# Kernel optimization log

Measured on AMD Instinct MI355X. Metric: run time of the kernel, lower is better.

Reference implementation:

```python
import jax, jax.numpy as jnp
import numpy as np

N_NODES = 100_000
N_EDGES = 1_600_000
F_IN = 128
HID = 64
C_OUT = 16


def setup_inputs() -> dict:
    key = jax.random.key(0)
    k1, k2, k3, k4, k5 = jax.random.split(key, 5)
    x = jax.random.normal(k1, (N_NODES, F_IN), dtype=jnp.float32)
    edge_index = jax.random.randint(k2, (2, N_EDGES), 0, N_NODES, dtype=jnp.int64)
    edge_weight = jax.random.uniform(k3, (N_EDGES,), dtype=jnp.float32)
    # Glorot-ish init for the two GCNConv linear layers; PyG inits bias to zero.
    W1 = jax.random.normal(k4, (F_IN, HID), dtype=jnp.float32) * (1.0 / np.sqrt(F_IN))
    b1 = jnp.zeros((HID,), dtype=jnp.float32)
    W2 = jax.random.normal(k5, (HID, C_OUT), dtype=jnp.float32) * (1.0 / np.sqrt(HID))
    b2 = jnp.zeros((C_OUT,), dtype=jnp.float32)
    return {"x": x, "edge_index": edge_index, "edge_weight": edge_weight,
            "W1": W1, "b1": b1, "W2": W2, "b2": b2}


def gcn_layer(x, row, col, ew, W, b, n):
    """PyG GCNConv: h = D^-1/2 (A + I) D^-1/2 (x W) + b, with edge weights.
    Self loops (weight 1) are handled analytically instead of appending edges."""
    h = x @ W  # [n, out]
    deg = jax.ops.segment_sum(ew, col, num_segments=n) + 1.0  # +1 for self loop
    dinv = jax.lax.rsqrt(deg)  # deg >= 1 always
    norm = dinv[row] * ew * dinv[col]  # [E]
    agg = jax.ops.segment_sum(norm[:, None] * h[row], col, num_segments=n)
    return agg + (dinv * dinv)[:, None] * h + b


def reference(x, edge_index, edge_weight, W1, b1, W2, b2):
    row, col = edge_index[0], edge_index[1]
    h = jax.nn.relu(gcn_layer(x, row, col, edge_weight, W1, b1, N_NODES))
    # delete_min_weighted_edges(node=0): remove the min-weight edge with source 0.
    # Zeroing its weight is mathematically identical to deleting it (it then
    # contributes 0 to both the degree and the aggregation).
    masked = jnp.where(row == 0, edge_weight, jnp.inf)
    idx = jnp.argmin(masked)
    ew2 = edge_weight.at[idx].set(0.0)
    return gcn_layer(h, row, col, ew2, W2, b2, N_NODES)
```

## Files before the change

kernel.cpp:

```cpp
#include <hip/hip_runtime.h>
#include <hip/hip_bf16.h>
#include <stdint.h>

#define NN 100000
#define NE 1600000
#define FIN 128
#define HID 64
#define COUT 16

#define BUKSH 8
#define BUKN 256
#define NBUK ((NN + BUKN - 1) >> BUKSH)
#define CAP 5120
#define PART_NB 200
#define EPB (NE / PART_NB)

typedef unsigned long long u64;
typedef short bf16x8 __attribute__((ext_vector_type(8)));
typedef float f32x4 __attribute__((ext_vector_type(4)));

struct Flags { int f32; int i64; };

__device__ __forceinline__ float b2f(__hip_bfloat16 v) { return __bfloat162float(v); }

__device__ __forceinline__ float ldf(const void* p, size_t i, int f32) {
    return f32 ? ((const float*)p)[i]
               : __bfloat162float(((const __hip_bfloat16*)p)[i]);
}
__device__ __forceinline__ int lde(const void* p, size_t i, int i64) {
    return i64 ? (int)((const long long*)p)[i] : ((const int*)p)[i];
}
__device__ __forceinline__ void ld4bf(const __hip_bfloat16* p, float& x0, float& x1,
                                      float& x2, float& x3) {
    union { uint2 u; __hip_bfloat16 h[4]; } v;
    v.u = *(const uint2*)p;
    x0 = b2f(v.h[0]); x1 = b2f(v.h[1]); x2 = b2f(v.h[2]); x3 = b2f(v.h[3]);
}
__device__ __forceinline__ unsigned short f2bfu(float f) {
    union { __hip_bfloat16 b; unsigned short u; } c;
    c.b = __float2bfloat16(f);
    return c.u;
}
__device__ __forceinline__ float bfu2f(unsigned short u) {
    union { unsigned short h[2]; float f; } c;
    c.h[0] = 0; c.h[1] = u;
    return c.f;
}

__global__ __launch_bounds__(256) void k_init(const unsigned short* xs,
                                              const int* ei32, Flags* fl,
                                              int* cursorA, u64* minkey,
                                              int* delpos) {
    int t = threadIdx.x;
    if (t < 64) {
        int lane = t;
        int huge = 0;
        for (int i = lane * 2; i < 1024; i += 128) {
            int e = (xs[i] >> 7) & 0xFF;
            if (e >= 0xC0) huge = 1;
        }
        int odd_nonzero = 0;
        for (int i = 1 + lane * 2; i < 512; i += 128) {
            if (ei32[i] != 0) odd_nonzero = 1;
        }
        u64 h = __ballot(huge), o = __ballot(odd_nonzero);
        if (lane == 0) { fl->f32 = (h != 0); fl->i64 = (o == 0); }
    }
    for (int i = t; i < NBUK; i += 256) cursorA[i] = 0;
    if (t == 64) *minkey = ~0ull;
    if (t == 65) *delpos = -1;
}

__global__ void k_mink(const void* __restrict__ ei, const void* __restrict__ ew,
                       const Flags* __restrict__ fl, u64* __restrict__ minkey) {
    int e = blockIdx.x * blockDim.x + threadIdx.x;
    if (e >= NE) return;
    int r = lde(ei, e, fl->i64);
    if (r == 0) {
        float w = ldf(ew, e, fl->f32);
        u64 key = ((u64)__float_as_uint(w) << 32) | (unsigned)e;
        atomicMin(minkey, key);
    }
}

__global__ __launch_bounds__(256) void k_partA(const void* __restrict__ ei,
                                               const void* __restrict__ ew,
                                               const Flags* __restrict__ fl,
                                               const u64* __restrict__ minkey,
                                               int* __restrict__ cursorA,
                                               long long* __restrict__ tmp) {
    __shared__ int cnt[NBUK];
    __shared__ int base[NBUK];
    int b = blockIdx.x, t = threadIdx.x;
    int f32 = fl->f32, i64 = fl->i64;
    for (int i = t; i < NBUK; i += 256) cnt[i] = 0;
    __syncthreads();
    int e0 = b * EPB;
    for (int i = t; i < EPB; i += 256) {
        int c = lde(ei, (size_t)NE + e0 + i, i64);
        atomicAdd(&cnt[c >> BUKSH], 1);
    }
    __syncthreads();
    for (int i = t; i < NBUK; i += 256) {
        int n = cnt[i];
        base[i] = n ? atomicAdd(&cursorA[i], n) : 0;
    }
    __syncthreads();
    for (int i = t; i < NBUK; i += 256) cnt[i] = 0;
    __syncthreads();
    u64 k = *minkey;
    int eidx = (k == ~0ull) ? 0 : (int)(k & 0xffffffffu);
    for (int i = t; i < EPB; i += 256) {
        int e = e0 + i;
        int r = lde(ei, e, i64);
        int c = lde(ei, (size_t)NE + e, i64);
        float w = ldf(ew, e, f32);
        int buk = c >> BUKSH;
        int slot = base[buk] + atomicAdd(&cnt[buk], 1);
        if (slot < CAP) {
            unsigned lo = (unsigned)r | (((unsigned)c & 255u) << 17)
                        | ((e == eidx) ? (1u << 25) : 0u);
            tmp[(size_t)buk * CAP + slot] = ((long long)__float_as_int(w) << 32) | lo;
        }
    }
}

__global__ __launch_bounds__(512) void k_scanBk(const int* __restrict__ cursorA,
                                                int* __restrict__ bucketBase,
                                                int* __restrict__ rowptrN) {
    __shared__ int sm[512];
    int t = threadIdx.x;
    int v = 0;
    if (t < NBUK) { v = cursorA[t]; if (v > CAP) v = CAP; }
    sm[t] = v;
    for (int off = 1; off < 512; off <<= 1) {
        __syncthreads();
        int add = (t >= off) ? sm[t - off] : 0;
        __syncthreads();
        sm[t] += add;
    }
    __syncthreads();
    if (t < NBUK) bucketBase[t] = sm[t] - v;
    if (t == 511) rowptrN[NN] = sm[511];
}

__global__ __launch_bounds__(256) void k_partB(const int* __restrict__ cursorA,
                                               const int* __restrict__ bucketBase,
                                               const long long* __restrict__ tmp,
                                               int2* __restrict__ epack,
                                               int* __restrict__ rowptrN,
                                               const void* __restrict__ ei,
                                               const void* __restrict__ ew,
                                               const Flags* __restrict__ fl,
                                               const u64* __restrict__ minkey,
                                               float* __restrict__ dinv1,
                                               float* __restrict__ dinv2,
                                               int* __restrict__ delpos) {
    __shared__ int cnt[256];
    __shared__ int pfx[256];
    __shared__ u64 wsum[256];
    int b = blockIdx.x, t = threadIdx.x;
    cnt[t] = 0; wsum[t] = 0;
    __syncthreads();
    int count = cursorA[b]; if (count > CAP) count = CAP;
    const long long* ts = tmp + (size_t)b * CAP;
    for (int i = t; i < count; i += 256) {
        long long pk = ts[i];
        unsigned lo = (unsigned)pk;
        int nl = (int)((lo >> 17) & 255u);
        atomicAdd(&cnt[nl], 1);
        float w = __int_as_float((int)(pk >> 32));
        atomicAdd(&wsum[nl], (u64)((double)w * 4294967296.0));
    }
    __syncthreads();
    int v = cnt[t];
    pfx[t] = v;
    for (int off = 1; off < 256; off <<= 1) {
        __syncthreads();
        int add = (t >= off) ? pfx[t - off] : 0;
        __syncthreads();
        pfx[t] += add;
    }
    __syncthreads();
    int excl = pfx[t] - v;
    int gbase = bucketBase[b];
    int node = (b << BUKSH) + t;
    if (node < NN) {
        rowptrN[node] = gbase + excl;
        float degv = (float)((double)wsum[t] * (1.0 / 4294967296.0));
        u64 kk = *minkey;
        int eidx = (kk == ~0ull) ? 0 : (int)(kk & 0xffffffffu);
        int cmin = lde(ei, (size_t)NE + eidx, fl->i64);
        float wmin = ldf(ew, eidx, fl->f32);
        float d1 = degv + 1.0f;
        float d2 = d1 - ((node == cmin) ? wmin : 0.0f);
        dinv1[node] = rsqrtf(d1);
        dinv2[node] = rsqrtf(d2);
    }
    __syncthreads();
    cnt[t] = gbase + excl;
    __syncthreads();
    for (int i = t; i < count; i += 256) {
        long long pk = ts[i];
        unsigned lo = (unsigned)pk;
        int nl = (int)((lo >> 17) & 255u);
        int pos = atomicAdd(&cnt[nl], 1);
        long long outpk = (pk & 0xFFFFFFFF00000000LL) | (lo & 0x1FFFFu);
        *(long long*)(epack + pos) = outpk;
        if (lo & (1u << 25)) *delpos = pos;
    }
}

__global__ __launch_bounds__(256, 3) void k_gemm1_split(const float* __restrict__ x,
                                                        const float* __restrict__ W1,
                                                        const Flags* __restrict__ fl,
                                                        const float* __restrict__ dinv1,
                                                        __hip_bfloat16* __restrict__ h1) {
    if (!fl->f32) return;
    __shared__ __align__(16) unsigned short Whi[8192];
    __shared__ __align__(16) unsigned short Wlo[8192];
    int t = threadIdx.x;
    for (int i = t; i < 8192; i += 256) {
        int k = i >> 6;
        int n = i & 63;
        int kc = k >> 5, kr = k & 31;
        int q = kr >> 3, j = kr & 7;
        int n0 = n >> 4, col = n & 15;
        float w = W1[i];
        unsigned short hi = f2bfu(w);
        unsigned short lo = f2bfu(w - bfu2f(hi));
        int idx = ((n0 << 4) + (kc << 2) + q) * 128 + col * 8 + j;
        Whi[idx] = hi;
        Wlo[idx] = lo;
    }
    __syncthreads();
    int wave = t >> 6, lane = t & 63;
    int quad = lane >> 4, col = lane & 15;
    bf16x8 Bh[4][4];
#pragma unroll
    for (int n0 = 0; n0 < 4; ++n0)
#pragma unroll
        for (int kc = 0; kc < 4; ++kc)
            Bh[kc][n0] = *(const bf16x8*)&Whi[((n0 << 4) + (kc << 2) + quad) * 128 + col * 8];
    int tile0 = (blockIdx.x * 4 + wave) * 2;
#pragma unroll 1
    for (int i = 0; i < 2; ++i) {
        int node0 = (tile0 + i) * 16;
        if (node0 >= NN) return;
        const float* xp = x + (size_t)(node0 + col) * FIN + quad * 8;
        float4 xv[8];
#pragma unroll
        for (int kc = 0; kc < 4; ++kc) {
            xv[2 * kc]     = *(const float4*)(xp + kc * 32);
            xv[2 * kc + 1] = *(const float4*)(xp + kc * 32 + 4);
        }
        f32x4 a0 = {0.f, 0.f, 0.f, 0.f}, a1 = a0, a2 = a0, a3 = a0;
#pragma unroll
        for (int kc = 0; kc < 4; ++kc) {
            float fv[8];
            fv[0] = xv[2 * kc].x;     fv[1] = xv[2 * kc].y;
            fv[2] = xv[2 * kc].z;     fv[3] = xv[2 * kc].w;
            fv[4] = xv[2 * kc + 1].x; fv[5] = xv[2 * kc + 1].y;
            fv[6] = xv[2 * kc + 1].z; fv[7] = xv[2 * kc + 1].w;
            bf16x8 Ah, Al;
#pragma unroll
            for (int j = 0; j < 8; ++j) {
                unsigned short hi = f2bfu(fv[j]);
                Ah[j] = (short)hi;
                Al[j] = (short)f2bfu(fv[j] - bfu2f(hi));
            }
            int lbase = ((kc << 2) + quad) * 128 + col * 8;
            bf16x8 Bl0 = *(const bf16x8*)&Wlo[lbase];
            bf16x8 Bl1 = *(const bf16x8*)&Wlo[(1 << 4) * 128 + lbase];
            bf16x8 Bl2 = *(const bf16x8*)&Wlo[(2 << 4) * 128 + lbase];
            bf16x8 Bl3 = *(const bf16x8*)&Wlo[(3 << 4) * 128 + lbase];
            a0 = __builtin_amdgcn_mfma_f32_16x16x32_bf16(Ah, Bh[kc][0], a0, 0, 0, 0);
            a0 = __builtin_amdgcn_mfma_f32_16x16x32_bf16(Al, Bh[kc][0], a0, 0, 0, 0);
            a0 = __builtin_amdgcn_mfma_f32_16x16x32_bf16(Ah, Bl0,      a0, 0, 0, 0);
            a1 = __builtin_amdgcn_mfma_f32_16x16x32_bf16(Ah, Bh[kc][1], a1, 0, 0, 0);
            a1 = __builtin_amdgcn_mfma_f32_16x16x32_bf16(Al, Bh[kc][1], a1, 0, 0, 0);
            a1 = __builtin_amdgcn_mfma_f32_16x16x32_bf16(Ah, Bl1,      a1, 0, 0, 0);
            a2 = __builtin_amdgcn_mfma_f32_16x16x32_bf16(Ah, Bh[kc][2], a2, 0, 0, 0);
            a2 = __builtin_amdgcn_mfma_f32_16x16x32_bf16(Al, Bh[kc][2], a2, 0, 0, 0);
            a2 = __builtin_amdgcn_mfma_f32_16x16x32_bf16(Ah, Bl2,      a2, 0, 0, 0);
            a3 = __builtin_amdgcn_mfma_f32_16x16x32_bf16(Ah, Bh[kc][3], a3, 0, 0, 0);
            a3 = __builtin_amdgcn_mfma_f32_16x16x32_bf16(Al, Bh[kc][3], a3, 0, 0, 0);
            a3 = __builtin_amdgcn_mfma_f32_16x16x32_bf16(Ah, Bl3,      a3, 0, 0, 0);
        }
        __hip_bfloat16* hp = h1 + (size_t)(node0 + quad * 4) * HID + col;
#pragma unroll
        for (int r = 0; r < 4; ++r) {
            float dsc = dinv1[node0 + quad * 4 + r];
            hp[(size_t)r * HID + 0]  = __float2bfloat16(a0[r] * dsc);
            hp[(size_t)r * HID + 16] = __float2bfloat16(a1[r] * dsc);
            hp[(size_t)r * HID + 32] = __float2bfloat16(a2[r] * dsc);
            hp[(size_t)r * HID + 48] = __float2bfloat16(a3[r] * dsc);
        }
    }
}

__global__ __launch_bounds__(256) void k_gemm1_mfma(const __hip_bfloat16* __restrict__ x,
                                                    const unsigned short* __restrict__ W1,
                                                    const Flags* __restrict__ fl,
                                                    const float* __restrict__ dinv1,
                                                    __hip_bfloat16* __restrict__ h1) {
    if (fl->f32) return;
    __shared__ __align__(16) unsigned short Wf[8192];
    int t = threadIdx.x;
    for (int i = t; i < 8192; i += 256) {
        int k = i >> 6;
        int n = i & 63;
        int kc = k >> 5, kr = k & 31;
        int q = kr >> 3, j = kr & 7;
        int n0 = n >> 4, col = n & 15;
        Wf[((((n0 << 2) | kc) << 2) | q) * 128 + col * 8 + j] = W1[i];
    }
    __syncthreads();
    int wave = t >> 6, lane = t & 63;
    int quad = lane >> 4, col = lane & 15;
    bf16x8 B[4][4];
#pragma unroll
    for (int n0 = 0; n0 < 4; ++n0)
#pragma unroll
        for (int kc = 0; kc < 4; ++kc)
            B[kc][n0] = *(const bf16x8*)&Wf[((((n0 << 2) | kc) << 2) | quad) * 128 + col * 8];
    int tile0 = (blockIdx.x * 4 + wave) * 4;
#pragma unroll 1
    for (int i = 0; i < 4; ++i) {
        int node0 = (tile0 + i) * 16;
        if (node0 >= NN) return;
        const __hip_bfloat16* xp = x + (size_t)(node0 + col) * FIN + quad * 8;
        f32x4 a0 = {0.f, 0.f, 0.f, 0.f}, a1 = a0, a2 = a0, a3 = a0;
#pragma unroll
        for (int kc = 0; kc < 4; ++kc) {
            bf16x8 A = *(const bf16x8*)(xp + kc * 32);
            a0 = __builtin_amdgcn_mfma_f32_16x16x32_bf16(A, B[kc][0], a0, 0, 0, 0);
            a1 = __builtin_amdgcn_mfma_f32_16x16x32_bf16(A, B[kc][1], a1, 0, 0, 0);
            a2 = __builtin_amdgcn_mfma_f32_16x16x32_bf16(A, B[kc][2], a2, 0, 0, 0);
            a3 = __builtin_amdgcn_mfma_f32_16x16x32_bf16(A, B[kc][3], a3, 0, 0, 0);
        }
        __hip_bfloat16* hp = h1 + (size_t)(node0 + quad * 4) * HID + col;
#pragma unroll
        for (int r = 0; r < 4; ++r) {
            float dsc = dinv1[node0 + quad * 4 + r];
            hp[(size_t)r * HID + 0]  = __float2bfloat16(a0[r] * dsc);
            hp[(size_t)r * HID + 16] = __float2bfloat16(a1[r] * dsc);
            hp[(size_t)r * HID + 32] = __float2bfloat16(a2[r] * dsc);
            hp[(size_t)r * HID + 48] = __float2bfloat16(a3[r] * dsc);
        }
    }
}

__global__ __launch_bounds__(256) void k_agg1(const int* __restrict__ rowptrN,
                                              const int2* __restrict__ epack,
                                              const float* __restrict__ dinv1,
                                              const __hip_bfloat16* __restrict__ h1,
                                              const void* __restrict__ b1,
                                              const void* __restrict__ W2,
                                              const Flags* __restrict__ fl,
                                              const float* __restrict__ dinv2,
                                              float* __restrict__ h2) {
    __shared__ float Ws[HID * COUT];
    __shared__ float obuf[16][68];
    int t = threadIdx.x;
    int f32 = fl->f32;
    for (int i = t; i < HID * COUT; i += 256) Ws[i] = ldf(W2, i, f32);
    int nn = t >> 4;
    int n = blockIdx.x * 16 + nn;
    int l = t & 15;
    int f = l * 4;
    int wbase = t & 48;
    float dn = dinv1[n];
    int p0 = rowptrN[n], p1 = rowptrN[n + 1];
    float a0 = 0.f, a1 = 0.f, a2 = 0.f, a3 = 0.f;
    for (int p = p0; p < p1; p += 16) {
        int idx = p + l;
        int2 ev = make_int2(0, 0);
        if (idx < p1) ev = epack[idx];
        float cw = __int_as_float(ev.y);
        int rj[16];
#pragma unroll
        for (int j = 0; j < 16; ++j)
            rj[j] = __shfl(ev.x, wbase + j);
        uint2 raw[16];
#pragma unroll
        for (int j = 0; j < 16; ++j)
            raw[j] = *(const uint2*)(h1 + (size_t)rj[j] * HID + f);
#pragma unroll
        for (int j = 0; j < 16; ++j) {
            float c = __shfl(cw, wbase + j);
            union { uint2 u; __hip_bfloat16 h[4]; } v; v.u = raw[j];
            a0 += c * b2f(v.h[0]);
            a1 += c * b2f(v.h[1]);
            a2 += c * b2f(v.h[2]);
            a3 += c * b2f(v.h[3]);
        }
    }
    float x0, x1, x2, x3;
    ld4bf(h1 + (size_t)n * HID + f, x0, x1, x2, x3);
    float4 o;
    o.x = fmaxf(dn * (a0 + x0) + ldf(b1, f + 0, f32), 0.f);
    o.y = fmaxf(dn * (a1 + x1) + ldf(b1, f + 1, f32), 0.f);
    o.z = fmaxf(dn * (a2 + x2) + ldf(b1, f + 2, f32), 0.f);
    o.w = fmaxf(dn * (a3 + x3) + ldf(b1, f + 3, f32), 0.f);
    obuf[nn][f + 0] = o.x; obuf[nn][f + 1] = o.y;
    obuf[nn][f + 2] = o.z; obuf[nn][f + 3] = o.w;
    __syncthreads();
    int c = t & 15;
    const float* orow = obuf[nn];
    float acc = 0.f;
#pragma unroll 8
    for (int k = 0; k < HID; ++k)
        acc += orow[k] * Ws[k * COUT + c];
    h2[(size_t)n * COUT + c] = acc * dinv2[n];
}

__global__ __launch_bounds__(256) void k_agg2(const int* __restrict__ rowptrN,
                                              const int2* __restrict__ epack,
                                              const float* __restrict__ dinv2,
                                              const float* __restrict__ h2,
                                              const void* __restrict__ bias2,
                                              const Flags* __restrict__ fl,
                                              const int* __restrict__ delpos,
                                              void* __restrict__ out) {
    int t = threadIdx.x;
    int n = blockIdx.x * 64 + (t >> 2);
    if (n >= NN) return;
    int l = t & 3;
    int f = l * 4;
    int wbase = t & 60;
    int f32 = fl->f32;
    int dp = *delpos;
    float dn = dinv2[n];
    int p0 = rowptrN[n], p1 = rowptrN[n + 1];
    float a0 = 0.f, a1 = 0.f, a2 = 0.f, a3 = 0.f;
    for (int p = p0; p < p1; p += 8) {
        int iA = p + l, iB = p + 4 + l;
        int2 evA = make_int2(0, 0), evB = make_int2(0, 0);
        if (iA < p1) evA = epack[iA];
        if (iB < p1) evB = epack[iB];
        float cwA = (iA == dp) ? 0.f : __int_as_float(evA.y);
        float cwB = (iB == dp) ? 0.f : __int_as_float(evB.y);
        int rj[8];
#pragma unroll
        for (int j = 0; j < 4; ++j) {
            rj[j]     = __shfl(evA.x, wbase + j);
            rj[4 + j] = __shfl(evB.x, wbase + j);
        }
        float4 hv[8];
#pragma unroll
        for (int j = 0; j < 8; ++j)
            hv[j] = *(const float4*)(h2 + (size_t)rj[j] * COUT + f);
#pragma unroll
        for (int j = 0; j < 4; ++j) {
            float cA = __shfl(cwA, wbase + j);
            float cB = __shfl(cwB, wbase + j);
            a0 += cA * hv[j].x + cB * hv[4 + j].x;
            a1 += cA * hv[j].y + cB * hv[4 + j].y;
            a2 += cA * hv[j].z + cB * hv[4 + j].z;
            a3 += cA * hv[j].w + cB * hv[4 + j].w;
        }
    }
    const float4 hn = *(const float4*)(h2 + (size_t)n * COUT + f);
    float o0 = dn * (a0 + hn.x) + ldf(bias2, f + 0, f32);
    float o1 = dn * (a1 + hn.y) + ldf(bias2, f + 1, f32);
    float o2 = dn * (a2 + hn.z) + ldf(bias2, f + 2, f32);
    float o3 = dn * (a3 + hn.w) + ldf(bias2, f + 3, f32);
    size_t idx = (size_t)n * COUT + f;
    if (f32) {
        float* op = (float*)out + idx;
        op[0] = o0; op[1] = o1; op[2] = o2; op[3] = o3;
    } else {
        union { uint2 u; __hip_bfloat16 h[4]; } pk;
        pk.h[0] = __float2bfloat16(o0); pk.h[1] = __float2bfloat16(o1);
        pk.h[2] = __float2bfloat16(o2); pk.h[3] = __float2bfloat16(o3);
        *(uint2*)((__hip_bfloat16*)out + idx) = pk.u;
    }
}

extern "C" void kernel_launch(void* const* d_in, const int* in_sizes, int n_in,
                              void* d_out, int out_size, void* d_ws, size_t ws_size,
                              hipStream_t stream) {
    const void* x  = d_in[0];
    const void* ei = d_in[1];
    const void* ew = d_in[2];
    const void* W1 = d_in[3];
    const void* b1 = d_in[4];
    const void* W2 = d_in[5];
    const void* b2 = d_in[6];

    char* wsb = (char*)d_ws;
    float* dinv1    = (float*)wsb;                     wsb += (size_t)NN * 4;
    float* dinv2    = (float*)wsb;                     wsb += (size_t)NN * 4;
    int*   rowptrN  = (int*)wsb;                       wsb += (size_t)(NN + 1) * 4;
    int*   cursorA  = (int*)wsb;                       wsb += (size_t)NBUK * 4;
    int*   bucketBase = (int*)wsb;                     wsb += (size_t)NBUK * 4;
    wsb = (char*)(((uintptr_t)wsb + 15) & ~(uintptr_t)15);
    int2*  epack    = (int2*)wsb;                      wsb += (size_t)NE * 8;
    __hip_bfloat16* h1 = (__hip_bfloat16*)wsb;         wsb += (size_t)NN * HID * 2;
    float* h2       = (float*)wsb;                     wsb += (size_t)NN * COUT * 4;
    long long* tmp  = (long long*)wsb;                 wsb += (size_t)NBUK * CAP * 8;
    u64*   minkey   = (u64*)wsb;                       wsb += 8;
    Flags* fl       = (Flags*)wsb;                     wsb += 8;
    int*   delpos   = (int*)wsb;                       wsb += 8;

    k_init<<<1, 256, 0, stream>>>((const unsigned short*)x, (const int*)ei, fl,
                                  cursorA, minkey, delpos);
    k_mink<<<(NE + 255) / 256, 256, 0, stream>>>(ei, ew, fl, minkey);
    k_partA<<<PART_NB, 256, 0, stream>>>(ei, ew, fl, minkey, cursorA, tmp);
    k_scanBk<<<1, 512, 0, stream>>>(cursorA, bucketBase, rowptrN);
    k_partB<<<NBUK, 256, 0, stream>>>(cursorA, bucketBase, tmp, epack, rowptrN,
                                      ei, ew, fl, minkey, dinv1, dinv2, delpos);
    k_gemm1_split<<<(NN / 16 + 7) / 8, 256, 0, stream>>>((const float*)x,
                                                         (const float*)W1, fl,
                                                         dinv1, h1);
    k_gemm1_mfma<<<(NN / 16 + 15) / 16, 256, 0, stream>>>((const __hip_bfloat16*)x,
                                                          (const unsigned short*)W1, fl,
                                                          dinv1, h1);
    k_agg1<<<NN / 16, 256, 0, stream>>>(rowptrN, epack, dinv1, h1, b1, W2, fl,
                                        dinv2, h2);
    k_agg2<<<(NN + 63) / 64, 256, 0, stream>>>(rowptrN, epack, dinv2, h2, b2, fl,
                                               delpos, d_out);
}
```

Baseline: 255.2 us.

## Fold bucket scan into partB, merge gemm kernels, widen agg1 loads

```diff
diff --git a/kernel.cpp b/kernel.cpp
--- a/kernel.cpp
+++ b/kernel.cpp
@@ -29,12 +29,6 @@
 }
 __device__ __forceinline__ int lde(const void* p, size_t i, int i64) {
     return i64 ? (int)((const long long*)p)[i] : ((const int*)p)[i];
-}
-__device__ __forceinline__ void ld4bf(const __hip_bfloat16* p, float& x0, float& x1,
-                                      float& x2, float& x3) {
-    union { uint2 u; __hip_bfloat16 h[4]; } v;
-    v.u = *(const uint2*)p;
-    x0 = b2f(v.h[0]); x1 = b2f(v.h[1]); x2 = b2f(v.h[2]); x3 = b2f(v.h[3]);
 }
 __device__ __forceinline__ unsigned short f2bfu(float f) {
     union { __hip_bfloat16 b; unsigned short u; } c;
@@ -68,7 +62,7 @@
     }
     for (int i = t; i < NBUK; i += 256) cursorA[i] = 0;
     if (t == 64) *minkey = ~0ull;
-    if (t == 65) *delpos = -1;
+    if (t == 65) *delpos = 0x7fffffff;
 }
 
 __global__ void k_mink(const void* __restrict__ ei, const void* __restrict__ ew,
@@ -86,7 +80,6 @@
 __global__ __launch_bounds__(256) void k_partA(const void* __restrict__ ei,
                                                const void* __restrict__ ew,
                                                const Flags* __restrict__ fl,
-                                               const u64* __restrict__ minkey,
                                                int* __restrict__ cursorA,
                                                long long* __restrict__ tmp) {
     __shared__ int cnt[NBUK];
@@ -108,8 +101,6 @@
     __syncthreads();
     for (int i = t; i < NBUK; i += 256) cnt[i] = 0;
     __syncthreads();
-    u64 k = *minkey;
-    int eidx = (k == ~0ull) ? 0 : (int)(k & 0xffffffffu);
     for (int i = t; i < EPB; i += 256) {
         int e = e0 + i;
         int r = lde(ei, e, i64);
@@ -118,34 +109,14 @@
         int buk = c >> BUKSH;
         int slot = base[buk] + atomicAdd(&cnt[buk], 1);
         if (slot < CAP) {
-            unsigned lo = (unsigned)r | (((unsigned)c & 255u) << 17)
-                        | ((e == eidx) ? (1u << 25) : 0u);
-            tmp[(size_t)buk * CAP + slot] = ((long long)__float_as_int(w) << 32) | lo;
-        }
-    }
-}
-
-__global__ __launch_bounds__(512) void k_scanBk(const int* __restrict__ cursorA,
-                                                int* __restrict__ bucketBase,
-                                                int* __restrict__ rowptrN) {
-    __shared__ int sm[512];
-    int t = threadIdx.x;
-    int v = 0;
-    if (t < NBUK) { v = cursorA[t]; if (v > CAP) v = CAP; }
-    sm[t] = v;
-    for (int off = 1; off < 512; off <<= 1) {
-        __syncthreads();
-        int add = (t >= off) ? sm[t - off] : 0;
-        __syncthreads();
-        sm[t] += add;
-    }
-    __syncthreads();
-    if (t < NBUK) bucketBase[t] = sm[t] - v;
-    if (t == 511) rowptrN[NN] = sm[511];
+            unsigned lo = (unsigned)r | (((unsigned)c & 255u) << 17);
+            long long rec = ((long long)__float_as_int(w) << 32) | lo;
+            __builtin_nontemporal_store(rec, &tmp[(size_t)buk * CAP + slot]);
+        }
+    }
 }
 
 __global__ __launch_bounds__(256) void k_partB(const int* __restrict__ cursorA,
-                                               const int* __restrict__ bucketBase,
                                                const long long* __restrict__ tmp,
                                                int2* __restrict__ epack,
                                                int* __restrict__ rowptrN,
@@ -160,12 +131,33 @@
     __shared__ int pfx[256];
     __shared__ u64 wsum[256];
     int b = blockIdx.x, t = threadIdx.x;
+    int partial = 0;
+    for (int i = t; i < NBUK; i += 256) {
+        int cc = cursorA[i]; if (cc > CAP) cc = CAP;
+        if (i < b) partial += cc;
+    }
+    pfx[t] = partial;
+    __syncthreads();
+    for (int off = 128; off > 0; off >>= 1) {
+        if (t < off) pfx[t] += pfx[t + off];
+        __syncthreads();
+    }
+    int gbase = pfx[0];
+    __syncthreads();
     cnt[t] = 0; wsum[t] = 0;
     __syncthreads();
     int count = cursorA[b]; if (count > CAP) count = CAP;
+    if (b == NBUK - 1 && t == 0) rowptrN[NN] = gbase + count;
+    u64 kk = *minkey;
+    int eidx = (kk == ~0ull) ? 0 : (int)(kk & 0xffffffffu);
+    int smin  = lde(ei, (size_t)eidx, fl->i64);
+    int cmin  = lde(ei, (size_t)NE + eidx, fl->i64);
+    int wminb = __float_as_int(ldf(ew, eidx, fl->f32));
+    bool myb = (b == (cmin >> BUKSH));
+    int clow = cmin & 255;
     const long long* ts = tmp + (size_t)b * CAP;
     for (int i = t; i < count; i += 256) {
-        long long pk = ts[i];
+        long long pk = __builtin_nontemporal_load(&ts[i]);
         unsigned lo = (unsigned)pk;
         int nl = (int)((lo >> 17) & 255u);
         atomicAdd(&cnt[nl], 1);
@@ -183,17 +175,12 @@
     }
     __syncthreads();
     int excl = pfx[t] - v;
-    int gbase = bucketBase[b];
     int node = (b << BUKSH) + t;
     if (node < NN) {
         rowptrN[node] = gbase + excl;
         float degv = (float)((double)wsum[t] * (1.0 / 4294967296.0));
-        u64 kk = *minkey;
-        int eidx = (kk == ~0ull) ? 0 : (int)(kk & 0xffffffffu);
-        int cmin = lde(ei, (size_t)NE + eidx, fl->i64);
-        float wmin = ldf(ew, eidx, fl->f32);
         float d1 = degv + 1.0f;
-        float d2 = d1 - ((node == cmin) ? wmin : 0.0f);
+        float d2 = d1 - ((node == cmin) ? __int_as_float(wminb) : 0.0f);
         dinv1[node] = rsqrtf(d1);
         dinv2[node] = rsqrtf(d2);
     }
@@ -201,152 +188,150 @@
     cnt[t] = gbase + excl;
     __syncthreads();
     for (int i = t; i < count; i += 256) {
-        long long pk = ts[i];
+        long long pk = __builtin_nontemporal_load(&ts[i]);
         unsigned lo = (unsigned)pk;
         int nl = (int)((lo >> 17) & 255u);
         int pos = atomicAdd(&cnt[nl], 1);
         long long outpk = (pk & 0xFFFFFFFF00000000LL) | (lo & 0x1FFFFu);
         *(long long*)(epack + pos) = outpk;
-        if (lo & (1u << 25)) *delpos = pos;
-    }
-}
-
-__global__ __launch_bounds__(256, 3) void k_gemm1_split(const float* __restrict__ x,
-                                                        const float* __restrict__ W1,
-                                                        const Flags* __restrict__ fl,
-                                                        const float* __restrict__ dinv1,
-                                                        __hip_bfloat16* __restrict__ h1) {
-    if (!fl->f32) return;
-    __shared__ __align__(16) unsigned short Whi[8192];
-    __shared__ __align__(16) unsigned short Wlo[8192];
+        if (myb && nl == clow && (int)(lo & 0x1FFFFu) == smin
+            && (int)(pk >> 32) == wminb)
+            atomicMin(delpos, pos);
+    }
+}
+
+__global__ __launch_bounds__(256, 3) void k_gemm1(const void* __restrict__ xv_,
+                                                  const void* __restrict__ W1_,
+                                                  const Flags* __restrict__ fl,
+                                                  const float* __restrict__ dinv1,
+                                                  __hip_bfloat16* __restrict__ h1) {
+    __shared__ __align__(16) unsigned short Wbuf[16384];
     int t = threadIdx.x;
-    for (int i = t; i < 8192; i += 256) {
-        int k = i >> 6;
-        int n = i & 63;
-        int kc = k >> 5, kr = k & 31;
-        int q = kr >> 3, j = kr & 7;
-        int n0 = n >> 4, col = n & 15;
-        float w = W1[i];
-        unsigned short hi = f2bfu(w);
-        unsigned short lo = f2bfu(w - bfu2f(hi));
-        int idx = ((n0 << 4) + (kc << 2) + q) * 128 + col * 8 + j;
-        Whi[idx] = hi;
-        Wlo[idx] = lo;
-    }
-    __syncthreads();
     int wave = t >> 6, lane = t & 63;
     int quad = lane >> 4, col = lane & 15;
-    bf16x8 Bh[4][4];
-#pragma unroll
-    for (int n0 = 0; n0 < 4; ++n0)
-#pragma unroll
-        for (int kc = 0; kc < 4; ++kc)
-            Bh[kc][n0] = *(const bf16x8*)&Whi[((n0 << 4) + (kc << 2) + quad) * 128 + col * 8];
-    int tile0 = (blockIdx.x * 4 + wave) * 2;
+    if (fl->f32) {
+        const float* x  = (const float*)xv_;
+        const float* W1 = (const float*)W1_;
+        unsigned short* Whi = Wbuf;
+        unsigned short* Wlo = Wbuf + 8192;
+        for (int i = t; i < 8192; i += 256) {
+            int k = i >> 6;
+            int n = i & 63;
+            int kc = k >> 5, kr = k & 31;
+            int q = kr >> 3, j = kr & 7;
+            int n0 = n >> 4, c2 = n & 15;
+            float w = W1[i];
+            unsigned short hi = f2bfu(w);
+            unsigned short lo = f2bfu(w - bfu2f(hi));
+            int idx = ((n0 << 4) + (kc << 2) + q) * 128 + c2 * 8 + j;
+            Whi[idx] = hi;
+            Wlo[idx] = lo;
+        }
+        __syncthreads();
+        bf16x8 Bh[4][4];
+#pragma unroll
+        for (int n0 = 0; n0 < 4; ++n0)
+#pragma unroll
+            for (int kc = 0; kc < 4; ++kc)
+                Bh[kc][n0] = *(const bf16x8*)&Whi[((n0 << 4) + (kc << 2) + quad) * 128 + col * 8];
+        int tile0 = (blockIdx.x * 4 + wave) * 2;
 #pragma unroll 1
-    for (int i = 0; i < 2; ++i) {
-        int node0 = (tile0 + i) * 16;
-        if (node0 >= NN) return;
-        const float* xp = x + (size_t)(node0 + col) * FIN + quad * 8;
-        float4 xv[8];
-#pragma unroll
-        for (int kc = 0; kc < 4; ++kc) {
-            xv[2 * kc]     = *(const float4*)(xp + kc * 32);
-            xv[2 * kc + 1] = *(const float4*)(xp + kc * 32 + 4);
-        }
-        f32x4 a0 = {0.f, 0.f, 0.f, 0.f}, a1 = a0, a2 = a0, a3 = a0;
-#pragma unroll
-        for (int kc = 0; kc < 4; ++kc) {
-            float fv[8];
-            fv[0] = xv[2 * kc].x;     fv[1] = xv[2 * kc].y;
-            fv[2] = xv[2 * kc].z;     fv[3] = xv[2 * kc].w;
-            fv[4] = xv[2 * kc + 1].x; fv[5] = xv[2 * kc + 1].y;
-            fv[6] = xv[2 * kc + 1].z; fv[7] = xv[2 * kc + 1].w;
-            bf16x8 Ah, Al;
-#pragma unroll
-            for (int j = 0; j < 8; ++j) {
-                unsigned short hi = f2bfu(fv[j]);
-                Ah[j] = (short)hi;
-                Al[j] = (short)f2bfu(fv[j] - bfu2f(hi));
+        for (int i = 0; i < 2; ++i) {
+            int node0 = (tile0 + i) * 16;
+            if (node0 >= NN) return;
+            const float* xp = x + (size_t)(node0 + col) * FIN + quad * 8;
+            float4 xv[8];
+#pragma unroll
+            for (int kc = 0; kc < 4; ++kc) {
+                xv[2 * kc]     = *(const float4*)(xp + kc * 32);
+                xv[2 * kc + 1] = *(const float4*)(xp + kc * 32 + 4);
             }
-            int lbase = ((kc << 2) + quad) * 128 + col * 8;
-            bf16x8 Bl0 = *(const bf16x8*)&Wlo[lbase];
-            bf16x8 Bl1 = *(const bf16x8*)&Wlo[(1 << 4) * 128 + lbase];
-            bf16x8 Bl2 = *(const bf16x8*)&Wlo[(2 << 4) * 128 + lbase];
-            bf16x8 Bl3 = *(const bf16x8*)&Wlo[(3 << 4) * 128 + lbase];
-            a0 = __builtin_amdgcn_mfma_f32_16x16x32_bf16(Ah, Bh[kc][0], a0, 0, 0, 0);
-            a0 = __builtin_amdgcn_mfma_f32_16x16x32_bf16(Al, Bh[kc][0], a0, 0, 0, 0);
-            a0 = __builtin_amdgcn_mfma_f32_16x16x32_bf16(Ah, Bl0,      a0, 0, 0, 0);
-            a1 = __builtin_amdgcn_mfma_f32_16x16x32_bf16(Ah, Bh[kc][1], a1, 0, 0, 0);
-            a1 = __builtin_amdgcn_mfma_f32_16x16x32_bf16(Al, Bh[kc][1], a1, 0, 0, 0);
-            a1 = __builtin_amdgcn_mfma_f32_16x16x32_bf16(Ah, Bl1,      a1, 0, 0, 0);
-            a2 = __builtin_amdgcn_mfma_f32_16x16x32_bf16(Ah, Bh[kc][2], a2, 0, 0, 0);
-            a2 = __builtin_amdgcn_mfma_f32_16x16x32_bf16(Al, Bh[kc][2], a2, 0, 0, 0);
-            a2 = __builtin_amdgcn_mfma_f32_16x16x32_bf16(Ah, Bl2,      a2, 0, 0, 0);
-            a3 = __builtin_amdgcn_mfma_f32_16x16x32_bf16(Ah, Bh[kc][3], a3, 0, 0, 0);
-            a3 = __builtin_amdgcn_mfma_f32_16x16x32_bf16(Al, Bh[kc][3], a3, 0, 0, 0);
-            a3 = __builtin_amdgcn_mfma_f32_16x16x32_bf16(Ah, Bl3,      a3, 0, 0, 0);
-        }
-        __hip_bfloat16* hp = h1 + (size_t)(node0 + quad * 4) * HID + col;
-#pragma unroll
-        for (int r = 0; r < 4; ++r) {
-            float dsc = dinv1[node0 + quad * 4 + r];
-            hp[(size_t)r * HID + 0]  = __float2bfloat16(a0[r] * dsc);
-            hp[(size_t)r * HID + 16] = __float2bfloat16(a1[r] * dsc);
-            hp[(size_t)r * HID + 32] = __float2bfloat16(a2[r] * dsc);
-            hp[(size_t)r * HID + 48] = __float2bfloat16(a3[r] * dsc);
-        }
-    }
-}
-
-__global__ __launch_bounds__(256) void k_gemm1_mfma(const __hip_bfloat16* __restrict__ x,
-                                                    const unsigned short* __restrict__ W1,
-                                                    const Flags* __restrict__ fl,
-                                                    const float* __restrict__ dinv1,
-                                                    __hip_bfloat16* __restrict__ h1) {
-    if (fl->f32) return;
-    __shared__ __align__(16) unsigned short Wf[8192];
-    int t = threadIdx.x;
-    for (int i = t; i < 8192; i += 256) {
-        int k = i >> 6;
-        int n = i & 63;
-        int kc = k >> 5, kr = k & 31;
-        int q = kr >> 3, j = kr & 7;
-        int n0 = n >> 4, col = n & 15;
-        Wf[((((n0 << 2) | kc) << 2) | q) * 128 + col * 8 + j] = W1[i];
-    }
-    __syncthreads();
-    int wave = t >> 6, lane = t & 63;
-    int quad = lane >> 4, col = lane & 15;
-    bf16x8 B[4][4];
-#pragma unroll
-    for (int n0 = 0; n0 < 4; ++n0)
-#pragma unroll
-        for (int kc = 0; kc < 4; ++kc)
-            B[kc][n0] = *(const bf16x8*)&Wf[((((n0 << 2) | kc) << 2) | quad) * 128 + col * 8];
-    int tile0 = (blockIdx.x * 4 + wave) * 4;
+            f32x4 a0 = {0.f, 0.f, 0.f, 0.f}, a1 = a0, a2 = a0, a3 = a0;
+#pragma unroll
+            for (int kc = 0; kc < 4; ++kc) {
+                float fv[8];
+                fv[0] = xv[2 * kc].x;     fv[1] = xv[2 * kc].y;
+                fv[2] = xv[2 * kc].z;     fv[3] = xv[2 * kc].w;
+                fv[4] = xv[2 * kc + 1].x; fv[5] = xv[2 * kc + 1].y;
+                fv[6] = xv[2 * kc + 1].z; fv[7] = xv[2 * kc + 1].w;
+                bf16x8 Ah, Al;
+#pragma unroll
+                for (int j = 0; j < 8; ++j) {
+                    unsigned short hi = f2bfu(fv[j]);
+                    Ah[j] = (short)hi;
+                    Al[j] = (short)f2bfu(fv[j] - bfu2f(hi));
+                }
+                int lbase = ((kc << 2) + quad) * 128 + col * 8;
+                bf16x8 Bl0 = *(const bf16x8*)&Wlo[lbase];
+                bf16x8 Bl1 = *(const bf16x8*)&Wlo[(1 << 4) * 128 + lbase];
+                bf16x8 Bl2 = *(const bf16x8*)&Wlo[(2 << 4) * 128 + lbase];
+                bf16x8 Bl3 = *(const bf16x8*)&Wlo[(3 << 4) * 128 + lbase];
+                a0 = __builtin_amdgcn_mfma_f32_16x16x32_bf16(Ah, Bh[kc][0], a0, 0, 0, 0);
+                a0 = __builtin_amdgcn_mfma_f32_16x16x32_bf16(Al, Bh[kc][0], a0, 0, 0, 0);
+                a0 = __builtin_amdgcn_mfma_f32_16x16x32_bf16(Ah, Bl0,      a0, 0, 0, 0);
+                a1 = __builtin_amdgcn_mfma_f32_16x16x32_bf16(Ah, Bh[kc][1], a1, 0, 0, 0);
+                a1 = __builtin_amdgcn_mfma_f32_16x16x32_bf16(Al, Bh[kc][1], a1, 0, 0, 0);
+                a1 = __builtin_amdgcn_mfma_f32_16x16x32_bf16(Ah, Bl1,      a1, 0, 0, 0);
+                a2 = __builtin_amdgcn_mfma_f32_16x16x32_bf16(Ah, Bh[kc][2], a2, 0, 0, 0);
+                a2 = __builtin_amdgcn_mfma_f32_16x16x32_bf16(Al, Bh[kc][2], a2, 0, 0, 0);
+                a2 = __builtin_amdgcn_mfma_f32_16x16x32_bf16(Ah, Bl2,      a2, 0, 0, 0);
+                a3 = __builtin_amdgcn_mfma_f32_16x16x32_bf16(Ah, Bh[kc][3], a3, 0, 0, 0);
+                a3 = __builtin_amdgcn_mfma_f32_16x16x32_bf16(Al, Bh[kc][3], a3, 0, 0, 0);
+                a3 = __builtin_amdgcn_mfma_f32_16x16x32_bf16(Ah, Bl3,      a3, 0, 0, 0);
+            }
+            __hip_bfloat16* hp = h1 + (size_t)(node0 + quad * 4) * HID + col;
+#pragma unroll
+            for (int r = 0; r < 4; ++r) {
+                float dsc = dinv1[node0 + quad * 4 + r];
+                hp[(size_t)r * HID + 0]  = __float2bfloat16(a0[r] * dsc);
+                hp[(size_t)r * HID + 16] = __float2bfloat16(a1[r] * dsc);
+                hp[(size_t)r * HID + 32] = __float2bfloat16(a2[r] * dsc);
+                hp[(size_t)r * HID + 48] = __float2bfloat16(a3[r] * dsc);
+            }
+        }
+    } else {
+        const __hip_bfloat16* x = (const __hip_bfloat16*)xv_;
+        const unsigned short* W1 = (const unsigned short*)W1_;
+        unsigned short* Wf = Wbuf;
+        for (int i = t; i < 8192; i += 256) {
+            int k = i >> 6;
+            int n = i & 63;
+            int kc = k >> 5, kr = k & 31;
+            int q = kr >> 3, j = kr & 7;
+            int n0 = n >> 4, c2 = n & 15;
+            Wf[((((n0 << 2) | kc) << 2) | q) * 128 + c2 * 8 + j] = W1[i];
+        }
+        __syncthreads();
+        bf16x8 B[4][4];
+#pragma unroll
+        for (int n0 = 0; n0 < 4; ++n0)
+#pragma unroll
+            for (int kc = 0; kc < 4; ++kc)
+                B[kc][n0] = *(const bf16x8*)&Wf[((((n0 << 2) | kc) << 2) | quad) * 128 + col * 8];
+        int tile0 = (blockIdx.x * 4 + wave) * 2;
 #pragma unroll 1
-    for (int i = 0; i < 4; ++i) {
-        int node0 = (tile0 + i) * 16;
-        if (node0 >= NN) return;
-        const __hip_bfloat16* xp = x + (size_t)(node0 + col) * FIN + quad * 8;
-        f32x4 a0 = {0.f, 0.f, 0.f, 0.f}, a1 = a0, a2 = a0, a3 = a0;
-#pragma unroll
-        for (int kc = 0; kc < 4; ++kc) {
-            bf16x8 A = *(const bf16x8*)(xp + kc * 32);
-            a0 = __builtin_amdgcn_mfma_f32_16x16x32_bf16(A, B[kc][0], a0, 0, 0, 0);
-            a1 = __builtin_amdgcn_mfma_f32_16x16x32_bf16(A, B[kc][1], a1, 0, 0, 0);
-            a2 = __builtin_amdgcn_mfma_f32_16x16x32_bf16(A, B[kc][2], a2, 0, 0, 0);
-            a3 = __builtin_amdgcn_mfma_f32_16x16x32_bf16(A, B[kc][3], a3, 0, 0, 0);
-        }
-        __hip_bfloat16* hp = h1 + (size_t)(node0 + quad * 4) * HID + col;
-#pragma unroll
-        for (int r = 0; r < 4; ++r) {
-            float dsc = dinv1[node0 + quad * 4 + r];
-            hp[(size_t)r * HID + 0]  = __float2bfloat16(a0[r] * dsc);
-            hp[(size_t)r * HID + 16] = __float2bfloat16(a1[r] * dsc);
-            hp[(size_t)r * HID + 32] = __float2bfloat16(a2[r] * dsc);
-            hp[(size_t)r * HID + 48] = __float2bfloat16(a3[r] * dsc);
+        for (int i = 0; i < 2; ++i) {
+            int node0 = (tile0 + i) * 16;
+            if (node0 >= NN) return;
+            const __hip_bfloat16* xp = x + (size_t)(node0 + col) * FIN + quad * 8;
+            f32x4 a0 = {0.f, 0.f, 0.f, 0.f}, a1 = a0, a2 = a0, a3 = a0;
+#pragma unroll
+            for (int kc = 0; kc < 4; ++kc) {
+                bf16x8 A = *(const bf16x8*)(xp + kc * 32);
+                a0 = __builtin_amdgcn_mfma_f32_16x16x32_bf16(A, B[kc][0], a0, 0, 0, 0);
+                a1 = __builtin_amdgcn_mfma_f32_16x16x32_bf16(A, B[kc][1], a1, 0, 0, 0);
+                a2 = __builtin_amdgcn_mfma_f32_16x16x32_bf16(A, B[kc][2], a2, 0, 0, 0);
+                a3 = __builtin_amdgcn_mfma_f32_16x16x32_bf16(A, B[kc][3], a3, 0, 0, 0);
+            }
+            __hip_bfloat16* hp = h1 + (size_t)(node0 + quad * 4) * HID + col;
+#pragma unroll
+            for (int r = 0; r < 4; ++r) {
+                float dsc = dinv1[node0 + quad * 4 + r];
+                hp[(size_t)r * HID + 0]  = __float2bfloat16(a0[r] * dsc);
+                hp[(size_t)r * HID + 16] = __float2bfloat16(a1[r] * dsc);
+                hp[(size_t)r * HID + 32] = __float2bfloat16(a2[r] * dsc);
+                hp[(size_t)r * HID + 48] = __float2bfloat16(a3[r] * dsc);
+            }
         }
     }
 }
@@ -361,58 +346,62 @@
                                               const float* __restrict__ dinv2,
                                               float* __restrict__ h2) {
     __shared__ float Ws[HID * COUT];
-    __shared__ float obuf[16][68];
+    __shared__ float obuf[32][65];
     int t = threadIdx.x;
     int f32 = fl->f32;
     for (int i = t; i < HID * COUT; i += 256) Ws[i] = ldf(W2, i, f32);
-    int nn = t >> 4;
-    int n = blockIdx.x * 16 + nn;
-    int l = t & 15;
-    int f = l * 4;
-    int wbase = t & 48;
+    int nn = t >> 3;
+    int l = t & 7;
+    int f = l * 8;
+    int wbase = t & 56;
+    int n = blockIdx.x * 32 + nn;
     float dn = dinv1[n];
     int p0 = rowptrN[n], p1 = rowptrN[n + 1];
-    float a0 = 0.f, a1 = 0.f, a2 = 0.f, a3 = 0.f;
-    for (int p = p0; p < p1; p += 16) {
+    float acc[8] = {0.f, 0.f, 0.f, 0.f, 0.f, 0.f, 0.f, 0.f};
+    for (int p = p0; p < p1; p += 8) {
         int idx = p + l;
-        int2 ev = make_int2(0, 0);
-        if (idx < p1) ev = epack[idx];
-        float cw = __int_as_float(ev.y);
-        int rj[16];
-#pragma unroll
-        for (int j = 0; j < 16; ++j)
-            rj[j] = __shfl(ev.x, wbase + j);
-        uint2 raw[16];
-#pragma unroll
-        for (int j = 0; j < 16; ++j)
-            raw[j] = *(const uint2*)(h1 + (size_t)rj[j] * HID + f);
-#pragma unroll
-        for (int j = 0; j < 16; ++j) {
+        long long pk = 0;
+        if (idx < p1)
+            pk = __builtin_nontemporal_load((const long long*)(epack + idx));
+        int src = (int)(unsigned)pk;
+        float cw = __int_as_float((int)(pk >> 32));
+        int rj[8];
+#pragma unroll
+        for (int j = 0; j < 8; ++j)
+            rj[j] = __shfl(src, wbase + j);
+        uint4 raw[8];
+#pragma unroll
+        for (int j = 0; j < 8; ++j)
+            raw[j] = *(const uint4*)(h1 + (size_t)rj[j] * HID + f);
+#pragma unroll
+        for (int j = 0; j < 8; ++j) {
             float c = __shfl(cw, wbase + j);
-            union { uint2 u; __hip_bfloat16 h[4]; } v; v.u = raw[j];
-            a0 += c * b2f(v.h[0]);
-            a1 += c * b2f(v.h[1]);
-            a2 += c * b2f(v.h[2]);
-            a3 += c * b2f(v.h[3]);
-        }
-    }
-    float x0, x1, x2, x3;
-    ld4bf(h1 + (size_t)n * HID + f, x0, x1, x2, x3);
-    float4 o;
-    o.x = fmaxf(dn * (a0 + x0) + ldf(b1, f + 0, f32), 0.f);
-    o.y = fmaxf(dn * (a1 + x1) + ldf(b1, f + 1, f32), 0.f);
-    o.z = fmaxf(dn * (a2 + x2) + ldf(b1, f + 2, f32), 0.f);
-    o.w = fmaxf(dn * (a3 + x3) + ldf(b1, f + 3, f32), 0.f);
-    obuf[nn][f + 0] = o.x; obuf[nn][f + 1] = o.y;
-    obuf[nn][f + 2] = o.z; obuf[nn][f + 3] = o.w;
+            union { uint4 u; unsigned short s[8]; } v; v.u = raw[j];
+#pragma unroll
+            for (int k = 0; k < 8; ++k) acc[k] += c * bfu2f(v.s[k]);
+        }
+    }
+    {
+        union { uint4 u; unsigned short s[8]; } sv;
+        sv.u = *(const uint4*)(h1 + (size_t)n * HID + f);
+#pragma unroll
+        for (int k = 0; k < 8; ++k)
+            obuf[nn][f + k] = fmaxf(dn * (acc[k] + bfu2f(sv.s[k]))
+                                    + ldf(b1, f + k, f32), 0.f);
+    }
     __syncthreads();
     int c = t & 15;
-    const float* orow = obuf[nn];
-    float acc = 0.f;
+#pragma unroll
+    for (int half = 0; half < 2; ++half) {
+        int nn2 = (t >> 4) + half * 16;
+        int node = blockIdx.x * 32 + nn2;
+        const float* orow = obuf[nn2];
+        float a = 0.f;
 #pragma unroll 8
-    for (int k = 0; k < HID; ++k)
-        acc += orow[k] * Ws[k * COUT + c];
-    h2[(size_t)n * COUT + c] = acc * dinv2[n];
+        for (int k = 0; k < HID; ++k)
+            a += orow[k] * Ws[k * COUT + c];
+        h2[(size_t)node * COUT + c] = a * dinv2[node];
+    }
 }
 
 __global__ __launch_bounds__(256) void k_agg2(const int* __restrict__ rowptrN,
@@ -436,16 +425,17 @@
     float a0 = 0.f, a1 = 0.f, a2 = 0.f, a3 = 0.f;
     for (int p = p0; p < p1; p += 8) {
         int iA = p + l, iB = p + 4 + l;
-        int2 evA = make_int2(0, 0), evB = make_int2(0, 0);
-        if (iA < p1) evA = epack[iA];
-        if (iB < p1) evB = epack[iB];
-        float cwA = (iA == dp) ? 0.f : __int_as_float(evA.y);
-        float cwB = (iB == dp) ? 0.f : __int_as_float(evB.y);
+        long long pkA = 0, pkB = 0;
+        if (iA < p1) pkA = __builtin_nontemporal_load((const long long*)(epack + iA));
+        if (iB < p1) pkB = __builtin_nontemporal_load((const long long*)(epack + iB));
+        int rA = (int)(unsigned)pkA, rB = (int)(unsigned)pkB;
+        float cwA = (iA == dp) ? 0.f : __int_as_float((int)(pkA >> 32));
+        float cwB = (iB == dp) ? 0.f : __int_as_float((int)(pkB >> 32));
         int rj[8];
 #pragma unroll
         for (int j = 0; j < 4; ++j) {
-            rj[j]     = __shfl(evA.x, wbase + j);
-            rj[4 + j] = __shfl(evB.x, wbase + j);
+            rj[j]     = __shfl(rA, wbase + j);
+            rj[4 + j] = __shfl(rB, wbase + j);
         }
         float4 hv[8];
 #pragma unroll
@@ -494,7 +484,6 @@
     float* dinv2    = (float*)wsb;                     wsb += (size_t)NN * 4;
     int*   rowptrN  = (int*)wsb;                       wsb += (size_t)(NN + 1) * 4;
     int*   cursorA  = (int*)wsb;                       wsb += (size_t)NBUK * 4;
-    int*   bucketBase = (int*)wsb;                     wsb += (size_t)NBUK * 4;
     wsb = (char*)(((uintptr_t)wsb + 15) & ~(uintptr_t)15);
     int2*  epack    = (int2*)wsb;                      wsb += (size_t)NE * 8;
     __hip_bfloat16* h1 = (__hip_bfloat16*)wsb;         wsb += (size_t)NN * HID * 2;
@@ -507,17 +496,11 @@
     k_init<<<1, 256, 0, stream>>>((const unsigned short*)x, (const int*)ei, fl,
                                   cursorA, minkey, delpos);
     k_mink<<<(NE + 255) / 256, 256, 0, stream>>>(ei, ew, fl, minkey);
-    k_partA<<<PART_NB, 256, 0, stream>>>(ei, ew, fl, minkey, cursorA, tmp);
-    k_scanBk<<<1, 512, 0, stream>>>(cursorA, bucketBase, rowptrN);
-    k_partB<<<NBUK, 256, 0, stream>>>(cursorA, bucketBase, tmp, epack, rowptrN,
+    k_partA<<<PART_NB, 256, 0, stream>>>(ei, ew, fl, cursorA, tmp);
+    k_partB<<<NBUK, 256, 0, stream>>>(cursorA, tmp, epack, rowptrN,
                                       ei, ew, fl, minkey, dinv1, dinv2, delpos);
-    k_gemm1_split<<<(NN / 16 + 7) / 8, 256, 0, stream>>>((const float*)x,
-                                                         (const float*)W1, fl,
-                                                         dinv1, h1);
-    k_gemm1_mfma<<<(NN / 16 + 15) / 16, 256, 0, stream>>>((const __hip_bfloat16*)x,
-                                                          (const unsigned short*)W1, fl,
-                                                          dinv1, h1);
-    k_agg1<<<NN / 16, 256, 0, stream>>>(rowptrN, epack, dinv1, h1, b1, W2, fl,
+    k_gemm1<<<(NN / 16 + 7) / 8, 256, 0, stream>>>(x, W1, fl, dinv1, h1);
+    k_agg1<<<NN / 32, 256, 0, stream>>>(rowptrN, epack, dinv1, h1, b1, W2, fl,
                                         dinv2, h2);
     k_agg2<<<(NN + 63) / 64, 256, 0, stream>>>(rowptrN, epack, dinv2, h2, b2, fl,
                                                delpos, d_out);
```

Result: slower. 311.8 us (+22.2%).
